# Performance work log

Measured on AMD Instinct MI355X. Metric: run time of the kernel, lower is better.

## Reference

```python
import jax, jax.numpy as jnp
import numpy as np

KS = 3; PAD = 1; NK = KS * KS  # 3x3 deform kernel, 9 sampling points

def conv2d(x, w, b=None, pad=1):
    out = jax.lax.conv_general_dilated(x, w, (1, 1), [(pad, pad), (pad, pad)],
                                       dimension_numbers=('NCHW', 'OIHW', 'NCHW'))
    return out if b is None else out + b[None, :, None, None]

def bn(x, g, b, m, v, eps=1e-5):
    s = g * jax.lax.rsqrt(v + eps)
    return x * s[None, :, None, None] + (b - m * s)[None, :, None, None]

def pool2(x, kind):
    if kind == 'max':
        return jax.lax.reduce_window(x, -jnp.inf, jax.lax.max, (1, 1, 2, 2), (1, 1, 2, 2), 'VALID')
    s = jax.lax.reduce_window(x, 0.0, jax.lax.add, (1, 1, 2, 2), (1, 1, 2, 2), 'VALID')
    return s * 0.25

def _gather(xflat, idx):
    # xflat [b,c,Hp*Wp], idx [b,h,w,NK] int32 -> [b,c,h,w,NK]
    b, c, _ = xflat.shape
    out = jax.vmap(lambda xf, ix: xf[:, ix])(xflat, idx.reshape(b, -1))
    return out.reshape(b, c, *idx.shape[1:])

def deform_conv(x, pw, pb, w):
    # DeformConv2D: internal offset conv -> bilinear gather -> 3x3-equivalent conv (einsum)
    b, c, h, wd = x.shape
    off = conv2d(x, pw, pb).transpose(0, 2, 3, 1)  # [b,h,w,2*NK], first NK = x(row), last NK = y(col)
    rng = jnp.arange(KS, dtype=x.dtype) - (KS - 1) // 2
    pn_x = jnp.repeat(rng, KS)  # kernel row offsets, n = 3*i + j ordering
    pn_y = jnp.tile(rng, KS)
    px = jnp.arange(1, h + 1, dtype=x.dtype)[:, None, None] + pn_x + off[..., :NK]  # [b,h,w,NK]
    py = jnp.arange(1, wd + 1, dtype=x.dtype)[None, :, None] + pn_y + off[..., NK:]
    Hp, Wp = h + 2 * PAD, wd + 2 * PAD
    px = jnp.clip(px, 0, Hp - 1); py = jnp.clip(py, 0, Wp - 1)
    x0 = jnp.clip(jnp.floor(px), 0, Hp - 1); y0 = jnp.clip(jnp.floor(py), 0, Wp - 1)
    x1 = jnp.clip(x0 + 1, 0, Hp - 1);        y1 = jnp.clip(y0 + 1, 0, Wp - 1)
    g_lt = (1 + x0 - px) * (1 + y0 - py)
    g_rb = (1 - x1 + px) * (1 - y1 + py)
    g_lb = (1 + x0 - px) * (1 - y1 + py)
    g_rt = (1 - x1 + px) * (1 + y0 - py)
    xp = jnp.pad(x, ((0, 0), (0, 0), (PAD, PAD), (PAD, PAD))).reshape(b, c, Hp * Wp)
    ix0 = x0.astype(jnp.int32); iy0 = y0.astype(jnp.int32)
    ix1 = x1.astype(jnp.int32); iy1 = y1.astype(jnp.int32)
    v = (g_lt[:, None] * _gather(xp, ix0 * Wp + iy0)
       + g_rb[:, None] * _gather(xp, ix1 * Wp + iy1)
       + g_lb[:, None] * _gather(xp, ix0 * Wp + iy1)
       + g_rt[:, None] * _gather(xp, ix1 * Wp + iy0))  # [b,c,h,w,NK]
    oc = w.shape[0]
    return jnp.einsum('bchwn,ocn->bohw', v, w.reshape(oc, c, NK))

def reference(x, d1_pw, d1_pb, d1_w, bn1_g, bn1_b, bn1_m, bn1_v,
              c2_w, c2_b, bn2_g, bn2_b, bn2_m, bn2_v,
              d3_pw, d3_pb, d3_w, bn3_g, bn3_b, bn3_m, bn3_v,
              c4_w, c4_b, bn4_g, bn4_b, bn4_m, bn4_v,
              c5_w, c5_b, bn5_g, bn5_b, bn5_m, bn5_v,
              c6_w, c6_b, bn6_g, bn6_b, bn6_m, bn6_v,
              fc_w, fc_b, fc1_w, fc1_b):
    h = jax.nn.relu(bn(deform_conv(x, d1_pw, d1_pb, d1_w), bn1_g, bn1_b, bn1_m, bn1_v))
    h = pool2(jax.nn.relu(bn(conv2d(h, c2_w, c2_b), bn2_g, bn2_b, bn2_m, bn2_v)), 'max')
    h = jax.nn.relu(bn(deform_conv(h, d3_pw, d3_pb, d3_w), bn3_g, bn3_b, bn3_m, bn3_v))  # Dropout(0.1) eval = id
    h = pool2(jax.nn.relu(bn(conv2d(h, c4_w, c4_b), bn4_g, bn4_b, bn4_m, bn4_v)), 'max')
    h = jax.nn.relu(bn(conv2d(h, c5_w, c5_b), bn5_g, bn5_b, bn5_m, bn5_v))
    h = pool2(jax.nn.relu(bn(conv2d(h, c6_w, c6_b), bn6_g, bn6_b, bn6_m, bn6_v)), 'avg')
    h = h.reshape(h.shape[0], -1)  # [b, 128*2*2]
    h = h @ fc_w.T + fc_b          # Dropout eval = id
    return h @ fc1_w.T + fc1_b

def setup_inputs():
    key = jax.random.key(0)
    keys = iter(jax.random.split(key, 80))
    nk = lambda: next(keys)
    B, C, P, NC = 128, 200, 16, 16
    d = {}
    d['x'] = jax.random.normal(nk(), (B, C, P, P), jnp.float32)
    def conv_w(oc, ic, k=3, scale=None):
        s = scale if scale is not None else 1.0 / np.sqrt(ic * k * k)
        return jax.random.normal(nk(), (oc, ic, k, k), jnp.float32) * s
    def add_bn(name, c):
        d[name + '_g'] = 1.0 + 0.1 * jax.random.normal(nk(), (c,), jnp.float32)
        d[name + '_b'] = 0.1 * jax.random.normal(nk(), (c,), jnp.float32)
        d[name + '_m'] = 0.1 * jax.random.normal(nk(), (c,), jnp.float32)
        d[name + '_v'] = jax.random.uniform(nk(), (c,), jnp.float32) + 0.5
    d['d1_pw'] = conv_w(2 * NK, C, scale=0.01); d['d1_pb'] = jnp.zeros(2 * NK, jnp.float32)
    d['d1_w'] = conv_w(96, C); add_bn('bn1', 96)
    d['c2_w'] = conv_w(96, 96); d['c2_b'] = jnp.zeros(96, jnp.float32); add_bn('bn2', 96)
    d['d3_pw'] = conv_w(2 * NK, 96, scale=0.01); d['d3_pb'] = jnp.zeros(2 * NK, jnp.float32)
    d['d3_w'] = conv_w(108, 96); add_bn('bn3', 108)
    d['c4_w'] = conv_w(108, 108); d['c4_b'] = jnp.zeros(108, jnp.float32); add_bn('bn4', 108)
    d['c5_w'] = conv_w(128, 108); d['c5_b'] = jnp.zeros(128, jnp.float32); add_bn('bn5', 128)
    d['c6_w'] = conv_w(128, 128); d['c6_b'] = jnp.zeros(128, jnp.float32); add_bn('bn6', 128)
    d['fc_w'] = jax.random.normal(nk(), (200, 512), jnp.float32) / np.sqrt(512)
    d['fc_b'] = jnp.zeros(200, jnp.float32)
    d['fc1_w'] = jax.random.normal(nk(), (NC, 200), jnp.float32) / np.sqrt(200)
    d['fc1_b'] = jnp.zeros(NC, jnp.float32)
    return d
```

## Files before the change

kernel.cpp:

```cpp
#include <hip/hip_runtime.h>

typedef __attribute__((ext_vector_type(8))) short short8;
typedef __attribute__((ext_vector_type(4))) float f32x4;

#define MFMA16(a, b, c) __builtin_amdgcn_mfma_f32_16x16x32_bf16(a, b, c, 0, 0, 0)

__device__ __forceinline__ unsigned short f2bf(float x) {
  union { float f; unsigned u; } c; c.f = x;
  unsigned r = c.u + 0x7FFFu + ((c.u >> 16) & 1u);
  return (unsigned short)(r >> 16);
}
__device__ __forceinline__ float bf2f(unsigned short h) {
  union { unsigned u; float f; } c; c.u = ((unsigned)h) << 16; return c.f;
}
__device__ __forceinline__ unsigned cvtpk(float lo, float hi) {
  unsigned r;
  asm("v_cvt_pk_bf16_f32 %0, %1, %2" : "=v"(r) : "v"(lo), "v"(hi));
  return r;
}

static constexpr size_t PK_D1PW = 0;
static constexpr size_t PK_D1W  = 122880;
static constexpr size_t PK_C2W  = 491520;
static constexpr size_t PK_D3PW = 663552;
static constexpr size_t PK_D3W  = 720896;
static constexpr size_t PK_C4W  = 921600;
static constexpr size_t OFF1_B  = 2269184;
static constexpr size_t H2P_B   = 2269184;
static constexpr size_t H1_B    = 5414912;
static constexpr size_t OFF3_B  = 5414912;
static constexpr size_t H3_B    = 5709824;
static constexpr size_t H4P_B   = 9248768;
static constexpr size_t H5_B    = 10133504;
static constexpr size_t H6P_B   = 11182080;
static constexpr size_t FCO_B   = 11444224;
static constexpr size_t PT5_B   = 11546624;
static constexpr size_t PT6_B   = 12044288;

__global__ __launch_bounds__(256) void k_pack6(
    const float* __restrict__ s0, const float* __restrict__ s1,
    const float* __restrict__ s2, const float* __restrict__ s3,
    const float* __restrict__ s4, const float* __restrict__ s5,
    char* __restrict__ ws) {
  int blk = blockIdx.x;
  const float* src; unsigned short* dst; int K, Kp, OC, IC;
  if      (blk <  240) { src=s0; dst=(unsigned short*)(ws+PK_D1PW); OC=18;  K=1800; Kp=1920; IC=200; }
  else if (blk <  960) { src=s1; dst=(unsigned short*)(ws+PK_D1W);  OC=96;  K=1800; Kp=1920; IC=200; blk -= 240; }
  else if (blk < 1296) { src=s2; dst=(unsigned short*)(ws+PK_C2W);  OC=96;  K=864;  Kp=896;  IC=96;  blk -= 960; }
  else if (blk < 1408) { src=s3; dst=(unsigned short*)(ws+PK_D3PW); OC=18;  K=864;  Kp=896;  IC=96;  blk -= 1296; }
  else if (blk < 1800) { src=s4; dst=(unsigned short*)(ws+PK_D3W);  OC=108; K=864;  Kp=896;  IC=96;  blk -= 1408; }
  else                 { src=s5; dst=(unsigned short*)(ws+PK_C4W);  OC=108; K=972;  Kp=1024; IC=108; blk -= 1800; }
  int e = blk * 256 + threadIdx.x;
  int oc = e / Kp, k = e - oc * Kp;
  float v = 0.f;
  if (oc < OC) {
    int NCB = (IC + 15) >> 4;
    if (k < NCB * 144) {
      int cb = k / 144, r = k - cb*144;
      int n = r >> 4, ci = cb*16 + (r & 15);
      if (ci < IC) v = src[(size_t)oc*K + ci*9 + n];
    }
  }
  dst[e] = f2bf(v);
}

__global__ __launch_bounds__(256) void k_packT(
    const float* __restrict__ s5, const float* __restrict__ s6,
    char* __restrict__ ws) {
  int e = blockIdx.x * 256 + threadIdx.x;
  if (e < 124416) {
    int k = e >> 7, oc = e & 127;
    ((float*)(ws + PT5_B))[e] = s5[(size_t)oc*972 + k];
  } else if (e < 124416 + 147456) {
    int e2 = e - 124416;
    int k = e2 >> 7, oc = e2 & 127;
    ((float*)(ws + PT6_B))[e2] = s6[(size_t)oc*1152 + k];
  }
}

template<int IC, int OC, int OCPAD, int NT, int H, int W, bool ROLLING,
         int MROWS = 64, int NSPL = 1>
__global__ __launch_bounds__(MROWS*4, 2) void k_dgemm(
    const float* __restrict__ in,
    const unsigned short* __restrict__ offb,
    const unsigned short* __restrict__ wpk,
    const float* __restrict__ bng, const float* __restrict__ bnb,
    const float* __restrict__ bnm, const float* __restrict__ bnv,
    float* __restrict__ out) {
  constexpr int NTH  = MROWS * 4;
  constexpr int HW   = H * W;
  constexpr int NCB  = (IC + 15) >> 4;
  constexpr int KV   = NCB * 144;
  constexpr int NP   = (KV + 63) / 64;
  constexpr int KPAD = NP * 64;
  constexpr int TILES = HW / MROWS;
  constexpr int HP = H + 2, WPD = W + 2;
  constexpr int BSZ = OCPAD * 64 * 2;
  constexpr int CHUNKF = HW * 16;
  constexpr int SLOTS  = ROLLING ? 2 : NCB;
  constexpr int XSZ    = SLOTS * CHUNKF * 4;
  constexpr int TBL  = MROWS * 9;
  constexpr int TIDX = TBL * 4, TWT = TBL * 16;
  constexpr int PBYTES = TIDX + TWT + BSZ + XSZ;
  constexpr int NBV = (OCPAD * 8 + NTH - 1) / NTH;
  __shared__ __align__(16) char pool[PBYTES];
  uchar4* s_idx = (uchar4*)pool;
  float4* s_wt  = (float4*)(pool + TIDX);
  unsigned short* s_bh = (unsigned short*)(pool + TIDX + TWT);
  float* s_xt = (float*)(pool + TIDX + TWT + BSZ);

  const int tid = threadIdx.x;
  const int grp = blockIdx.x % (TILES * NSPL);
  const int b   = blockIdx.x / (TILES * NSPL);
  const int hw0 = (grp / NSPL) * MROWS;
  const int ns  = grp % NSPL;
  const int oc0 = ns * OCPAD;
  const unsigned short* __restrict__ wpk_s = wpk + (size_t)oc0 * KPAD;
  const float* __restrict__ inb = in + (size_t)b * IC * HW;

  for (int i = tid; i < TBL; i += NTH) {
    int px2 = i / 9, n = i % 9;
    int h = (hw0 + px2) / W, w = (hw0 + px2) % W;
    float offx = bf2f(offb[(((size_t)b*18 + n)*HW) + h*W + w]);
    float offy = bf2f(offb[(((size_t)b*18 + 9 + n)*HW) + h*W + w]);
    float pxv = (float)(h + n/3) + offx;
    float pyv = (float)(w + n%3) + offy;
    pxv = fminf(fmaxf(pxv, 0.f), (float)(HP - 1));
    pyv = fminf(fmaxf(pyv, 0.f), (float)(WPD - 1));
    float x0 = floorf(pxv), y0 = floorf(pyv);
    float x1 = fminf(x0 + 1.f, (float)(HP - 1));
    float y1 = fminf(y0 + 1.f, (float)(WPD - 1));
    float glt = (1.f + x0 - pxv) * (1.f + y0 - pyv);
    float grb = (1.f - x1 + pxv) * (1.f - y1 + pyv);
    float glb = (1.f + x0 - pxv) * (1.f - y1 + pyv);
    float grt = (1.f - x1 + pxv) * (1.f + y0 - pyv);
    int   cx[4] = {(int)x0, (int)x1, (int)x0, (int)x1};
    int   cy[4] = {(int)y0, (int)y1, (int)y1, (int)y0};
    float gw[4] = {glt, grb, glb, grt};
    unsigned char id[4]; float gg[4];
#pragma unroll
    for (int q = 0; q < 4; ++q) {
      bool ok = (cx[q] >= 1) && (cx[q] <= H) && (cy[q] >= 1) && (cy[q] <= W);
      id[q] = ok ? (unsigned char)((cx[q]-1)*W + (cy[q]-1)) : (unsigned char)0;
      gg[q] = ok ? gw[q] : 0.f;
    }
    s_idx[i] = make_uchar4(id[0], id[1], id[2], id[3]);
    s_wt[i]  = make_float4(gg[0], gg[1], gg[2], gg[3]);
  }

  auto stageX = [&](int cb) {
    const int slot = ROLLING ? (cb & 1) : cb;
    float* dst = s_xt + (size_t)slot * CHUNKF;
    for (int u = tid; u < HW * 4; u += NTH) {
      const int pp = u & (HW - 1);
      const int qj = u / HW;
      float4 v4;
#pragma unroll
      for (int i2 = 0; i2 < 4; ++i2) {
        int ci = cb*16 + qj*4 + i2;
        ((float*)&v4)[i2] = (ci < IC) ? inb[(size_t)ci*HW + pp] : 0.f;
      }
      *(float4*)(dst + pp*16 + ((((pp >> 1) + qj) & 3) << 2)) = v4;
    }
  };
  if (ROLLING) stageX(0);
  else { for (int cb = 0; cb < NCB; ++cb) stageX(cb); }
  int staged = 0;

  const int lane = tid & 63;
  const int wv   = tid >> 6;
  const int m16  = lane & 15;
  const int quad = lane >> 4;
  const int pv   = wv*16 + m16;
  const int tbase = pv * 9;
  f32x4 acc[NT];
#pragma unroll
  for (int nt = 0; nt < NT; ++nt) acc[nt] = (f32x4){0.f, 0.f, 0.f, 0.f};
  short8 rb[NBV];

  auto prefB = [&](int p) {
    if (p >= NP) return;
    const int k0 = p * 64;
#pragma unroll
    for (int j = 0; j < NBV; ++j) {
      int e = tid + NTH*j;
      if (e < OCPAD*8) {
        int oc = e >> 3, kq = e & 7;
        rb[j] = *(const short8*)(wpk_s + (size_t)oc*KPAD + k0 + kq*8);
      }
    }
  };
  auto commitB = [&]() {
#pragma unroll
    for (int j = 0; j < NBV; ++j) {
      int e = tid + NTH*j;
      if (e < OCPAD*8) {
        int oc = e >> 3, kq = e & 7;
        *(short8*)&s_bh[(kq*OCPAD + (oc ^ ((kq*2)&7)))*8] = rb[j];
      }
    }
  };

  auto buildA = [&](int kk, short8& ahv, short8& alv) {
    float v[8];
    if (kk < KV) {
      const int cb2 = kk / 144;
      const int rem = kk - cb2*144;
      const int n   = rem >> 4;
      const int g0  = (rem >> 2) & 2;
      const int slot = ROLLING ? (cb2 & 1) : cb2;
      const float* xb = s_xt + (size_t)slot * CHUNKF;
      uchar4 t4 = s_idx[tbase + n];
      float4 w4 = s_wt[tbase + n];
      const int r0i = (int)t4.x, r1i = (int)t4.y;
      const int r2i = (int)t4.z, r3i = (int)t4.w;
      const float* r0 = xb + r0i * 16;
      const float* r1 = xb + r1i * 16;
      const float* r2 = xb + r2i * 16;
      const float* r3 = xb + r3i * 16;
      float4 A0[2], A1[2], A2[2], A3[2];
#pragma unroll
      for (int j = 0; j < 2; ++j) {
        A0[j] = *(const float4*)(r0 + ((((r0i >> 1) + g0 + j) & 3) << 2));
        A1[j] = *(const float4*)(r1 + ((((r1i >> 1) + g0 + j) & 3) << 2));
        A2[j] = *(const float4*)(r2 + ((((r2i >> 1) + g0 + j) & 3) << 2));
        A3[j] = *(const float4*)(r3 + ((((r3i >> 1) + g0 + j) & 3) << 2));
      }
#pragma unroll
      for (int j = 0; j < 2; ++j) {
        v[4*j+0] = w4.x*A0[j].x + w4.y*A1[j].x + w4.z*A2[j].x + w4.w*A3[j].x;
        v[4*j+1] = w4.x*A0[j].y + w4.y*A1[j].y + w4.z*A2[j].y + w4.w*A3[j].y;
        v[4*j+2] = w4.x*A0[j].z + w4.y*A1[j].z + w4.z*A2[j].z + w4.w*A3[j].z;
        v[4*j+3] = w4.x*A0[j].w + w4.y*A1[j].w + w4.z*A2[j].w + w4.w*A3[j].w;
      }
    } else {
#pragma unroll
      for (int i = 0; i < 8; ++i) v[i] = 0.f;
    }
    unsigned hp[4], lp[4];
#pragma unroll
    for (int i = 0; i < 4; ++i) {
      unsigned h = cvtpk(v[2*i], v[2*i+1]);
      float h0 = __uint_as_float(h << 16);
      float h1 = __uint_as_float(h & 0xFFFF0000u);
      hp[i] = h;
      lp[i] = cvtpk(v[2*i] - h0, v[2*i+1] - h1);
    }
    uint4 uh = make_uint4(hp[0], hp[1], hp[2], hp[3]);
    uint4 ul = make_uint4(lp[0], lp[1], lp[2], lp[3]);
    ahv = *(short8*)&uh;
    alv = *(short8*)&ul;
  };

  prefB(0);
  __syncthreads();

  for (int p = 0; p < NP; ++p) {
    short8 ah[2], al[2];
    buildA(p*64 +      quad*8, ah[0], al[0]);
    buildA(p*64 + 32 + quad*8, ah[1], al[1]);
    commitB();
    if (ROLLING) {
      int want = ((p + 1) * 64 + 63) / 144;
      if (want >= NCB) want = NCB - 1;
      if (want > staged) { stageX(want); staged = want; }
    }
    prefB(p + 1);
    __syncthreads();
#pragma unroll
    for (int ks = 0; ks < 2; ++ks) {
      const int kg = ks*4 + quad;
      const int xm = (kg*2) & 7;
#pragma unroll
      for (int nt = 0; nt < NT; ++nt) {
        short8 bh = *(const short8*)&s_bh[(kg*OCPAD + ((nt*16 + m16) ^ xm))*8];
        acc[nt] = MFMA16(ah[ks], bh, acc[nt]);
        acc[nt] = MFMA16(al[ks], bh, acc[nt]);
      }
    }
    __syncthreads();
  }

#pragma unroll
  for (int nt = 0; nt < NT; ++nt) {
    int oc = oc0 + nt*16 + m16;
    if (oc < OC) {
      float sc = bng[oc] * rsqrtf(bnv[oc] + 1e-5f);
      float sh = bnb[oc] - bnm[oc] * sc;
#pragma unroll
      for (int reg = 0; reg < 4; ++reg) {
        int rowl = wv*16 + quad*4 + reg;
        float e = fmaxf(acc[nt][reg] * sc + sh, 0.f);
        out[((size_t)b*OC + oc)*HW + hw0 + rowl] = e;
      }
    }
  }
}

template<int IC, int OC, int OCPAD, int NT, int H, int W,
         bool HASBIAS, bool HASBN, bool RELU, int OUTMODE, int MINW, bool ALO>
__global__ __launch_bounds__(256, MINW) void k_gemm(
    const float* __restrict__ in,
    const unsigned short* __restrict__ wpk,
    const float* __restrict__ bias,
    const float* __restrict__ bng, const float* __restrict__ bnb,
    const float* __restrict__ bnm, const float* __restrict__ bnv,
    void* __restrict__ outv) {
  constexpr int HW   = H * W;
  constexpr int NCB  = (IC + 15) >> 4;
  constexpr int KV   = NCB * 144;
  constexpr int NP   = (KV + 63) / 64;
  constexpr int KPAD = NP * 64;
  constexpr int TILES = HW / 64;
  constexpr int RT   = 64 / W;
  constexpr int HR   = RT + 2, WPD = W + 2;
  constexpr int HPOS = HR * WPD;
  constexpr int SROW = 20;
  constexpr int CHUNKF = HPOS * SROW;
  constexpr int XSZ  = 2 * CHUNKF * 4;
  constexpr int BSLOT = OCPAD * 64;
  constexpr int BSZ  = 2 * BSLOT * 2;
  constexpr int PBST = BSZ + XSZ;
  constexpr int SOUTB = (OUTMODE == 2) ? 64 * (OC + 1) * 4 : 0;
  constexpr int PBYTES = (PBST > SOUTB) ? PBST : SOUTB;
  constexpr int NBV = (OCPAD * 8 + 255) / 256;
  __shared__ __align__(16) char pool[PBYTES];
  unsigned short* s_bh = (unsigned short*)pool;
  float* s_xt  = (float*)(pool + BSZ);
  float* s_out = (float*)pool;

  const int tid = threadIdx.x;
  const int b   = blockIdx.x / TILES;
  const int hw0 = (blockIdx.x % TILES) * 64;
  const int r0  = hw0 / W;
  const float* __restrict__ inb = in + (size_t)b * IC * HW;

  const int lane = tid & 63;
  const int wv   = tid >> 6;
  const int m16  = lane & 15;
  const int quad = lane >> 4;
  const int pv   = wv*16 + m16;
  const int lr   = pv / W, lc = pv % W;
  f32x4 acc[NT];
#pragma unroll
  for (int nt = 0; nt < NT; ++nt) acc[nt] = (f32x4){0.f, 0.f, 0.f, 0.f};
  short8 rb[NBV];

  auto stageX = [&](int cb) {
    float* dst = s_xt + (size_t)(cb & 1) * CHUNKF;
    for (int e = tid; e < HPOS * 4; e += 256) {
      int pos = e >> 2, g = e & 3;
      int hr = pos / WPD, hc = pos % WPD;
      int ir = r0 + hr - 1, ic = hc - 1;
      bool okp = (ir >= 0) && (ir < H) && (ic >= 0) && (ic < W);
      float4 v4;
#pragma unroll
      for (int i2 = 0; i2 < 4; ++i2) {
        int ci = cb*16 + g*4 + i2;
        ((float*)&v4)[i2] = (okp && ci < IC) ? inb[(size_t)ci*HW + ir*W + ic] : 0.f;
      }
      *(float4*)(dst + (size_t)pos*SROW + g*4) = v4;
    }
  };

  auto prefB = [&](int p) {
    if (p >= NP) return;
    const int k0 = p * 64;
#pragma unroll
    for (int j = 0; j < NBV; ++j) {
      int e = tid + 256*j;
      if (e < OCPAD*8) {
        int oc = e >> 3, kq = e & 7;
        rb[j] = *(const short8*)(wpk + (size_t)oc*KPAD + k0 + kq*8);
      }
    }
  };
  auto commitB = [&](int slot) {
    unsigned short* sb = s_bh + (size_t)slot * BSLOT;
#pragma unroll
    for (int j = 0; j < NBV; ++j) {
      int e = tid + 256*j;
      if (e < OCPAD*8) {
        int oc = e >> 3, kq = e & 7;
        *(short8*)&sb[(kq*OCPAD + (oc ^ ((kq*2)&7)))*8] = rb[j];
      }
    }
  };

  auto buildV = [&](int kk, short8& ahv, short8& alv) {
    float v[8];
    if (kk < KV) {
      const int cb2 = kk / 144;
      const int rem = kk - cb2*144;
      const int n   = rem >> 4;
      const int g0  = (rem >> 2) & 2;
      const float* xb = s_xt + (size_t)(cb2 & 1) * CHUNKF;
      const int hpos = (lr + n/3) * WPD + (lc + n%3);
      const float* rowp = xb + (size_t)hpos * SROW;
      float4 a0 = *(const float4*)(rowp + g0*4);
      float4 a1 = *(const float4*)(rowp + (g0+1)*4);
      v[0]=a0.x; v[1]=a0.y; v[2]=a0.z; v[3]=a0.w;
      v[4]=a1.x; v[5]=a1.y; v[6]=a1.z; v[7]=a1.w;
    } else {
#pragma unroll
      for (int i = 0; i < 8; ++i) v[i] = 0.f;
    }
    unsigned hp[4], lp[4];
#pragma unroll
    for (int i = 0; i < 4; ++i) {
      unsigned h = cvtpk(v[2*i], v[2*i+1]);
      hp[i] = h;
      if constexpr (ALO) {
        float h0 = __uint_as_float(h << 16);
        float h1 = __uint_as_float(h & 0xFFFF0000u);
        lp[i] = cvtpk(v[2*i] - h0, v[2*i+1] - h1);
      }
    }
    uint4 uh = make_uint4(hp[0], hp[1], hp[2], hp[3]);
    ahv = *(short8*)&uh;
    if constexpr (ALO) {
      uint4 ul = make_uint4(lp[0], lp[1], lp[2], lp[3]);
      alv = *(short8*)&ul;
    }
  };

  stageX(0);
  prefB(0);
  int staged = 0;
  __syncthreads();

  for (int p = 0; p < NP; ++p) {
    short8 ah[2], al[2];
    buildV(p*64 +      quad*8, ah[0], al[0]);
    buildV(p*64 + 32 + quad*8, ah[1], al[1]);
    commitB(p & 1);
    prefB(p + 1);
    {
      int want = ((p + 1) * 64 + 63) / 144;
      if (want >= NCB) want = NCB - 1;
      if (want > staged) { stageX(want); staged = want; }
    }
    __syncthreads();
    const unsigned short* sb = s_bh + (size_t)(p & 1) * BSLOT;
#pragma unroll
    for (int ks = 0; ks < 2; ++ks) {
      const int kg = ks*4 + quad;
      const int xm = (kg*2) & 7;
#pragma unroll
      for (int nt = 0; nt < NT; ++nt) {
        short8 bh = *(const short8*)&sb[(kg*OCPAD + ((nt*16 + m16) ^ xm))*8];
        acc[nt] = MFMA16(ah[ks], bh, acc[nt]);
        if constexpr (ALO) acc[nt] = MFMA16(al[ks], bh, acc[nt]);
      }
    }
  }

  constexpr int OCS = OC + 1;
  if constexpr (OUTMODE == 2) {
    __syncthreads();
  }
#pragma unroll
  for (int nt = 0; nt < NT; ++nt) {
    int oc = nt*16 + m16;
    float bi = 0.f, sc = 1.f, sh = 0.f;
    if (oc < OC) {
      if constexpr (HASBIAS) bi = bias[oc];
      if constexpr (HASBN) {
        sc = bng[oc] * rsqrtf(bnv[oc] + 1e-5f);
        sh = bnb[oc] - bnm[oc] * sc;
      }
    }
#pragma unroll
    for (int reg = 0; reg < 4; ++reg) {
      int rowl = wv*16 + quad*4 + reg;
      float e = (acc[nt][reg] + bi) * sc + sh;
      if constexpr (RELU) e = fmaxf(e, 0.f);
      if (oc < OC) {
        if constexpr (OUTMODE == 1) {
          ((unsigned short*)outv)[((size_t)b*OC + oc)*HW + hw0 + rowl] = f2bf(e);
        } else {
          s_out[rowl*OCS + oc] = e;
        }
      }
    }
  }
  if constexpr (OUTMODE == 2) {
    __syncthreads();
    constexpr int PR = (64 / W) / 2, PC = W / 2, CNT = PR * PC * OC;
    float* out = (float*)outv;
    for (int e2 = tid; e2 < CNT; e2 += 256) {
      int oc = e2 % OC, q = e2 / OC, pc2 = q % PC, pr2 = q / PC;
      int base = ((2*pr2)*W + 2*pc2)*OCS + oc;
      float a0 = s_out[base],         a1 = s_out[base + OCS];
      float a2 = s_out[base + W*OCS], a3 = s_out[base + W*OCS + OCS];
      float m = fmaxf(fmaxf(a0, a1), fmaxf(a2, a3));
      out[(((size_t)b*OC + oc)*(H/2) + (r0 >> 1) + pr2)*(W/2) + pc2] = m;
    }
  }
}

template<int IC, int OC, bool POOLAVG>
__global__ __launch_bounds__(256, 4) void k_tail(
    const float* __restrict__ in,
    const float* __restrict__ wt,
    const float* __restrict__ bias,
    const float* __restrict__ bng, const float* __restrict__ bnb,
    const float* __restrict__ bnm, const float* __restrict__ bnv,
    float* __restrict__ out) {
  constexpr int NB = OC / 32;
  __shared__ float s_pad[IC * 36];
  const int tid = threadIdx.x;
  const int b = blockIdx.x / NB;
  const int g = blockIdx.x % NB;
  for (int i = tid; i < IC*36; i += 256) {
    int ci = i / 36, pos = i % 36;
    int rr = pos / 6 - 1, cc = pos % 6 - 1;
    bool ok = (rr >= 0) && (rr < 4) && (cc >= 0) && (cc < 4);
    s_pad[i] = ok ? in[((size_t)b*IC + ci)*16 + rr*4 + cc] : 0.f;
  }
  __syncthreads();
  const int oc = g*32 + (tid >> 3);
  const int p  = tid & 7;
  const int r0 = p >> 1, c0 = (p & 1) * 2;
  float a0 = 0.f, a1 = 0.f;
  const float* wp = wt + oc;
#pragma unroll 2
  for (int ci = 0; ci < IC; ++ci) {
    const float* sp = s_pad + ci*36 + r0*6 + c0;
#pragma unroll
    for (int n = 0; n < 9; ++n) {
      float wv = wp[(size_t)(ci*9 + n)*OC];
      float v0 = sp[(n/3)*6 + (n%3)];
      float v1 = sp[(n/3)*6 + (n%3) + 1];
      a0 = fmaf(wv, v0, a0);
      a1 = fmaf(wv, v1, a1);
    }
  }
  float sc = bng[oc] * rsqrtf(bnv[oc] + 1e-5f);
  float sh = bnb[oc] - bnm[oc]*sc;
  float bi = bias[oc];
  float e0 = fmaxf((a0 + bi)*sc + sh, 0.f);
  float e1 = fmaxf((a1 + bi)*sc + sh, 0.f);
  if constexpr (!POOLAVG) {
    size_t ob = ((size_t)b*OC + oc)*16 + r0*4 + c0;
    out[ob]     = e0;
    out[ob + 1] = e1;
  } else {
    float s = e0 + e1;
    float tot = s + __shfl_xor(s, 2);
    if ((p & 2) == 0) {
      int pr = p >> 2, pc = p & 1;
      out[(size_t)b*512 + oc*4 + pr*2 + pc] = tot * 0.25f;
    }
  }
}

__global__ __launch_bounds__(128) void k_fc(const float* __restrict__ in,
                                            const float* __restrict__ w,
                                            const float* __restrict__ bias,
                                            float* __restrict__ out) {
  int j = blockIdx.x, b = threadIdx.x;
  const float4* ib = (const float4*)(in + (size_t)b*512);
  const float4* wb = (const float4*)(w + (size_t)j*512);
  float acc = bias[j];
  for (int k = 0; k < 128; ++k) {
    float4 a = ib[k], q = wb[k];
    acc = fmaf(a.x, q.x, fmaf(a.y, q.y, fmaf(a.z, q.z, fmaf(a.w, q.w, acc))));
  }
  out[(size_t)b*200 + j] = acc;
}

__global__ __launch_bounds__(128) void k_fc1(const float* __restrict__ in,
                                             const float* __restrict__ w,
                                             const float* __restrict__ bias,
                                             float* __restrict__ out) {
  int j = blockIdx.x, b = threadIdx.x;
  const float4* ib = (const float4*)(in + (size_t)b*200);
  const float4* wb = (const float4*)(w + (size_t)j*200);
  float acc = bias[j];
  for (int k = 0; k < 50; ++k) {
    float4 a = ib[k], q = wb[k];
    acc = fmaf(a.x, q.x, fmaf(a.y, q.y, fmaf(a.z, q.z, fmaf(a.w, q.w, acc))));
  }
  out[(size_t)b*16 + j] = acc;
}

extern "C" void kernel_launch(void* const* d_in, const int* in_sizes, int n_in,
                              void* d_out, int out_size, void* d_ws, size_t ws_size,
                              hipStream_t stream) {
  const float* X    = (const float*)d_in[0];
  const float* D1PW = (const float*)d_in[1];
  const float* D1PB = (const float*)d_in[2];
  const float* D1W  = (const float*)d_in[3];
  const float* BN1G = (const float*)d_in[4];
  const float* BN1B = (const float*)d_in[5];
  const float* BN1M = (const float*)d_in[6];
  const float* BN1V = (const float*)d_in[7];
  const float* C2W  = (const float*)d_in[8];
  const float* C2B  = (const float*)d_in[9];
  const float* BN2G = (const float*)d_in[10];
  const float* BN2B = (const float*)d_in[11];
  const float* BN2M = (const float*)d_in[12];
  const float* BN2V = (const float*)d_in[13];
  const float* D3PW = (const float*)d_in[14];
  const float* D3PB = (const float*)d_in[15];
  const float* D3W  = (const float*)d_in[16];
  const float* BN3G = (const float*)d_in[17];
  const float* BN3B = (const float*)d_in[18];
  const float* BN3M = (const float*)d_in[19];
  const float* BN3V = (const float*)d_in[20];
  const float* C4W  = (const float*)d_in[21];
  const float* C4B  = (const float*)d_in[22];
  const float* BN4G = (const float*)d_in[23];
  const float* BN4B = (const float*)d_in[24];
  const float* BN4M = (const float*)d_in[25];
  const float* BN4V = (const float*)d_in[26];
  const float* C5W  = (const float*)d_in[27];
  const float* C5B  = (const float*)d_in[28];
  const float* BN5G = (const float*)d_in[29];
  const float* BN5B = (const float*)d_in[30];
  const float* BN5M = (const float*)d_in[31];
  const float* BN5V = (const float*)d_in[32];
  const float* C6W  = (const float*)d_in[33];
  const float* C6B  = (const float*)d_in[34];
  const float* BN6G = (const float*)d_in[35];
  const float* BN6B = (const float*)d_in[36];
  const float* BN6M = (const float*)d_in[37];
  const float* BN6V = (const float*)d_in[38];
  const float* FCW  = (const float*)d_in[39];
  const float* FCB  = (const float*)d_in[40];
  const float* FC1W = (const float*)d_in[41];
  const float* FC1B = (const float*)d_in[42];

  char* ws = (char*)d_ws;
  unsigned short* pk_d1pw = (unsigned short*)(ws + PK_D1PW);
  unsigned short* pk_d1w  = (unsigned short*)(ws + PK_D1W);
  unsigned short* pk_c2w  = (unsigned short*)(ws + PK_C2W);
  unsigned short* pk_d3pw = (unsigned short*)(ws + PK_D3PW);
  unsigned short* pk_d3w  = (unsigned short*)(ws + PK_D3W);
  unsigned short* pk_c4w  = (unsigned short*)(ws + PK_C4W);
  unsigned short* off1 = (unsigned short*)(ws + OFF1_B);
  unsigned short* off3 = (unsigned short*)(ws + OFF3_B);
  float* h1   = (float*)(ws + H1_B);
  float* h2p  = (float*)(ws + H2P_B);
  float* h3   = (float*)(ws + H3_B);
  float* h4p  = (float*)(ws + H4P_B);
  float* h5   = (float*)(ws + H5_B);
  float* h6p  = (float*)(ws + H6P_B);
  float* fco  = (float*)(ws + FCO_B);
  float* pt5  = (float*)(ws + PT5_B);
  float* pt6  = (float*)(ws + PT6_B);
  float* outp = (float*)d_out;

  k_pack6<<<2248, 256, 0, stream>>>(D1PW, D1W, C2W, D3PW, D3W, C4W, ws);

  k_gemm<200,18,32,2,16,16,true,false,false,1,3,false><<<512, 256, 0, stream>>>(
      X, pk_d1pw, D1PB, nullptr, nullptr, nullptr, nullptr, off1);
  k_dgemm<200,96,48,3,16,16,true,128,2><<<512, 512, 0, stream>>>(
      X, off1, pk_d1w, BN1G, BN1B, BN1M, BN1V, h1);
  k_gemm<96,96,96,6,16,16,true,true,true,2,3,true><<<512, 256, 0, stream>>>(
      h1, pk_c2w, C2B, BN2G, BN2B, BN2M, BN2V, h2p);
  k_packT<<<1062, 256, 0, stream>>>(C5W, C6W, ws);
  k_gemm<96,18,32,2,8,8,true,false,false,1,3,false><<<128, 256, 0, stream>>>(
      h2p, pk_d3pw, D3PB, nullptr, nullptr, nullptr, nullptr, off3);
  k_dgemm<96,108,112,7,8,8,false><<<128, 256, 0, stream>>>(
      h2p, off3, pk_d3w, BN3G, BN3B, BN3M, BN3V, h3);
  k_gemm<108,108,112,7,8,8,true,true,true,2,3,true><<<128, 256, 0, stream>>>(
      h3, pk_c4w, C4B, BN4G, BN4B, BN4M, BN4V, h4p);
  k_tail<108,128,false><<<512, 256, 0, stream>>>(
      h4p, pt5, C5B, BN5G, BN5B, BN5M, BN5V, h5);
  k_tail<128,128,true><<<512, 256, 0, stream>>>(
      h5, pt6, C6B, BN6G, BN6B, BN6M, BN6V, h6p);
  k_fc<<<200, 128, 0, stream>>>(h6p, FCW, FCB, fco);
  k_fc1<<<16, 128, 0, stream>>>(fco, FC1W, FC1B, outp);
}
```

Before: 439.0 us.

## Split output channels across blocks for small-spatial layers, unsplit first dgemm

Adds an NSPL template parameter to the GEMM kernel so one spatial tile's output channels are divided across several blocks, each loading its own slice of packed weights. The 8x8 layers (offset conv, second deform conv, conv4) now launch 256 blocks instead of 128, which fills more of the GPU's compute units. The first deform GEMM goes the other way, from a 2-way split to a single 96-channel block with half as many blocks. Weight packing is enlarged to hold the padded channel splits. The cost is duplicated staging of input tiles across the split blocks.

```diff
diff --git a/kernel.cpp b/kernel.cpp
--- a/kernel.cpp
+++ b/kernel.cpp
@@ -24,7 +24,7 @@
 static constexpr size_t PK_C2W  = 491520;
 static constexpr size_t PK_D3PW = 663552;
 static constexpr size_t PK_D3W  = 720896;
-static constexpr size_t PK_C4W  = 921600;
+static constexpr size_t PK_C4W  = 950272;
 static constexpr size_t OFF1_B  = 2269184;
 static constexpr size_t H2P_B   = 2269184;
 static constexpr size_t H1_B    = 5414912;
@@ -48,8 +48,8 @@
   else if (blk <  960) { src=s1; dst=(unsigned short*)(ws+PK_D1W);  OC=96;  K=1800; Kp=1920; IC=200; blk -= 240; }
   else if (blk < 1296) { src=s2; dst=(unsigned short*)(ws+PK_C2W);  OC=96;  K=864;  Kp=896;  IC=96;  blk -= 960; }
   else if (blk < 1408) { src=s3; dst=(unsigned short*)(ws+PK_D3PW); OC=18;  K=864;  Kp=896;  IC=96;  blk -= 1296; }
-  else if (blk < 1800) { src=s4; dst=(unsigned short*)(ws+PK_D3W);  OC=108; K=864;  Kp=896;  IC=96;  blk -= 1408; }
-  else                 { src=s5; dst=(unsigned short*)(ws+PK_C4W);  OC=108; K=972;  Kp=1024; IC=108; blk -= 1800; }
+  else if (blk < 1856) { src=s4; dst=(unsigned short*)(ws+PK_D3W);  OC=108; K=864;  Kp=896;  IC=96;  blk -= 1408; }
+  else                 { src=s5; dst=(unsigned short*)(ws+PK_C4W);  OC=108; K=972;  Kp=1024; IC=108; blk -= 1856; }
   int e = blk * 256 + threadIdx.x;
   int oc = e / Kp, k = e - oc * Kp;
   float v = 0.f;
@@ -298,7 +298,8 @@
 }
 
 template<int IC, int OC, int OCPAD, int NT, int H, int W,
-         bool HASBIAS, bool HASBN, bool RELU, int OUTMODE, int MINW, bool ALO>
+         bool HASBIAS, bool HASBN, bool RELU, int OUTMODE, int MINW, bool ALO,
+         int NSPL = 1>
 __global__ __launch_bounds__(256, MINW) void k_gemm(
     const float* __restrict__ in,
     const unsigned short* __restrict__ wpk,
@@ -321,7 +322,7 @@
   constexpr int BSLOT = OCPAD * 64;
   constexpr int BSZ  = 2 * BSLOT * 2;
   constexpr int PBST = BSZ + XSZ;
-  constexpr int SOUTB = (OUTMODE == 2) ? 64 * (OC + 1) * 4 : 0;
+  constexpr int SOUTB = (OUTMODE == 2) ? 64 * (OCPAD + 1) * 4 : 0;
   constexpr int PBYTES = (PBST > SOUTB) ? PBST : SOUTB;
   constexpr int NBV = (OCPAD * 8 + 255) / 256;
   __shared__ __align__(16) char pool[PBYTES];
@@ -330,8 +331,12 @@
   float* s_out = (float*)pool;
 
   const int tid = threadIdx.x;
-  const int b   = blockIdx.x / TILES;
-  const int hw0 = (blockIdx.x % TILES) * 64;
+  const int grp = blockIdx.x % (TILES * NSPL);
+  const int b   = blockIdx.x / (TILES * NSPL);
+  const int hw0 = (grp / NSPL) * 64;
+  const int ns  = grp % NSPL;
+  const int oc0 = ns * OCPAD;
+  const unsigned short* __restrict__ wpk_s = wpk + (size_t)oc0 * KPAD;
   const int r0  = hw0 / W;
   const float* __restrict__ inb = in + (size_t)b * IC * HW;
 
@@ -371,7 +376,7 @@
       int e = tid + 256*j;
       if (e < OCPAD*8) {
         int oc = e >> 3, kq = e & 7;
-        rb[j] = *(const short8*)(wpk + (size_t)oc*KPAD + k0 + kq*8);
+        rb[j] = *(const short8*)(wpk_s + (size_t)oc*KPAD + k0 + kq*8);
       }
     }
   };
@@ -455,13 +460,14 @@
     }
   }
 
-  constexpr int OCS = OC + 1;
+  constexpr int OCS = OCPAD + 1;
   if constexpr (OUTMODE == 2) {
     __syncthreads();
   }
 #pragma unroll
   for (int nt = 0; nt < NT; ++nt) {
-    int oc = nt*16 + m16;
+    int ocl = nt*16 + m16;
+    int oc  = oc0 + ocl;
     float bi = 0.f, sc = 1.f, sh = 0.f;
     if (oc < OC) {
       if constexpr (HASBIAS) bi = bias[oc];
@@ -479,22 +485,24 @@
         if constexpr (OUTMODE == 1) {
           ((unsigned short*)outv)[((size_t)b*OC + oc)*HW + hw0 + rowl] = f2bf(e);
         } else {
-          s_out[rowl*OCS + oc] = e;
+          s_out[rowl*OCS + ocl] = e;
         }
       }
     }
   }
   if constexpr (OUTMODE == 2) {
     __syncthreads();
-    constexpr int PR = (64 / W) / 2, PC = W / 2, CNT = PR * PC * OC;
+    constexpr int PR = (64 / W) / 2, PC = W / 2;
+    const int OCL = (OC - oc0 < OCPAD) ? (OC - oc0) : OCPAD;
+    const int CNT = PR * PC * OCL;
     float* out = (float*)outv;
     for (int e2 = tid; e2 < CNT; e2 += 256) {
-      int oc = e2 % OC, q = e2 / OC, pc2 = q % PC, pr2 = q / PC;
-      int base = ((2*pr2)*W + 2*pc2)*OCS + oc;
+      int ocl = e2 % OCL, q = e2 / OCL, pc2 = q % PC, pr2 = q / PC;
+      int base = ((2*pr2)*W + 2*pc2)*OCS + ocl;
       float a0 = s_out[base],         a1 = s_out[base + OCS];
       float a2 = s_out[base + W*OCS], a3 = s_out[base + W*OCS + OCS];
       float m = fmaxf(fmaxf(a0, a1), fmaxf(a2, a3));
-      out[(((size_t)b*OC + oc)*(H/2) + (r0 >> 1) + pr2)*(W/2) + pc2] = m;
+      out[(((size_t)b*OC + oc0 + ocl)*(H/2) + (r0 >> 1) + pr2)*(W/2) + pc2] = m;
     }
   }
 }
@@ -652,20 +660,20 @@
   float* pt6  = (float*)(ws + PT6_B);
   float* outp = (float*)d_out;
 
-  k_pack6<<<2248, 256, 0, stream>>>(D1PW, D1W, C2W, D3PW, D3W, C4W, ws);
+  k_pack6<<<2368, 256, 0, stream>>>(D1PW, D1W, C2W, D3PW, D3W, C4W, ws);
 
   k_gemm<200,18,32,2,16,16,true,false,false,1,3,false><<<512, 256, 0, stream>>>(
       X, pk_d1pw, D1PB, nullptr, nullptr, nullptr, nullptr, off1);
-  k_dgemm<200,96,48,3,16,16,true,128,2><<<512, 512, 0, stream>>>(
+  k_dgemm<200,96,96,6,16,16,true,128><<<256, 512, 0, stream>>>(
       X, off1, pk_d1w, BN1G, BN1B, BN1M, BN1V, h1);
   k_gemm<96,96,96,6,16,16,true,true,true,2,3,true><<<512, 256, 0, stream>>>(
       h1, pk_c2w, C2B, BN2G, BN2B, BN2M, BN2V, h2p);
   k_packT<<<1062, 256, 0, stream>>>(C5W, C6W, ws);
-  k_gemm<96,18,32,2,8,8,true,false,false,1,3,false><<<128, 256, 0, stream>>>(
+  k_gemm<96,18,16,1,8,8,true,false,false,1,3,false,2><<<256, 256, 0, stream>>>(
       h2p, pk_d3pw, D3PB, nullptr, nullptr, nullptr, nullptr, off3);
-  k_dgemm<96,108,112,7,8,8,false><<<128, 256, 0, stream>>>(
+  k_dgemm<96,108,64,4,8,8,false,64,2><<<256, 256, 0, stream>>>(
       h2p, off3, pk_d3w, BN3G, BN3B, BN3M, BN3V, h3);
-  k_gemm<108,108,112,7,8,8,true,true,true,2,3,true><<<128, 256, 0, stream>>>(
+  k_gemm<108,108,64,4,8,8,true,true,true,2,3,true,2><<<256, 256, 0, stream>>>(
       h3, pk_c4w, C4B, BN4G, BN4B, BN4M, BN4V, h4p);
   k_tail<108,128,false><<<512, 256, 0, stream>>>(
       h4p, pt5, C5B, BN5G, BN5B, BN5M, BN5V, h5);
```

After: 403.9 us, median of 2. 8.0% less time.
